# Kernel optimization log

Hardware: AMD Instinct MI355X
Metric: run time of the kernel (lower is better)

Reference implementation:

```python
import jax, jax.numpy as jnp
import numpy as np

F_CONST = 1.0
B_CONST = 0.1
R_CONST = 0.01
N, DIM = 8192, 64


def setup_inputs() -> dict:
    key = jax.random.key(0)
    k1, k2 = jax.random.split(key)
    x = jax.random.uniform(k1, (N, DIM), dtype=jnp.float32)
    A = jax.random.uniform(k2, (N, N), dtype=jnp.float32)
    return {"t": 0, "x": x, "A": A}


def reference(t, x, A):
    # dx_i/dt = f - b*x_i - diag(A @ (r * x x^T))
    # diag(A @ (x x^T))[i] = sum_j A_ij <x_j, x_i> = <x_i, (A x)_i>
    Ax = A @ x                                      # [N, DIM]
    outer = R_CONST * jnp.sum(x * Ax, axis=1, keepdims=True)  # [N, 1]
    return F_CONST - B_CONST * x - outer            # broadcasts to [N, DIM]
```

## Files before the change

### kernel.cpp

```cpp
#include <hip/hip_runtime.h>

#define N 8192
#define DIM 64

typedef float f32x4 __attribute__((ext_vector_type(4)));
typedef short bf16x8 __attribute__((ext_vector_type(8)));

__device__ __forceinline__ unsigned short f32_to_bf16_rne(float f) {
  unsigned int u = __float_as_uint(f);
  unsigned int r = (u + 0x7FFFu + ((u >> 16) & 1u)) >> 16;
  return (unsigned short)r;
}

__global__ void cvt_kernel(const float* __restrict__ x, unsigned short* __restrict__ xb) {
  int gid = blockIdx.x * blockDim.x + threadIdx.x;
  float4 v = reinterpret_cast<const float4*>(x)[gid];
  ushort4 o;
  o.x = f32_to_bf16_rne(v.x);
  o.y = f32_to_bf16_rne(v.y);
  o.z = f32_to_bf16_rne(v.z);
  o.w = f32_to_bf16_rne(v.w);
  reinterpret_cast<ushort4*>(xb)[gid] = o;
}

__global__ void main_kernel(const float* __restrict__ A,
                            const unsigned short* __restrict__ xb,
                            float* __restrict__ spart) {
  int bid = blockIdx.x;
  int rg = bid & 127;
  int js = bid >> 7;
  int tid = threadIdx.x;
  int w = tid >> 6;
  int lane = tid & 63;
  int i0 = rg * 64;
  int jbase = js * 1024 + w * 256;
  int c = lane & 15;
  int q = lane >> 4;

  bf16x8 xi[4][2];
#pragma unroll
  for (int it = 0; it < 4; ++it)
#pragma unroll
    for (int kb = 0; kb < 2; ++kb)
      xi[it][kb] = *reinterpret_cast<const bf16x8*>(
          xb + (size_t)(i0 + it * 16 + c) * DIM + kb * 32 + q * 8);

  float sacc[4][4] = {};

  for (int jt = 0; jt < 16; ++jt) {
    int jcol = jbase + jt * 16;
    bf16x8 xj0 = *reinterpret_cast<const bf16x8*>(
        xb + (size_t)(jcol + c) * DIM + q * 8);
    bf16x8 xj1 = *reinterpret_cast<const bf16x8*>(
        xb + (size_t)(jcol + c) * DIM + 32 + q * 8);

    float a[4][4];
#pragma unroll
    for (int it = 0; it < 4; ++it)
#pragma unroll
      for (int v = 0; v < 4; ++v)
        a[it][v] = A[(size_t)(i0 + it * 16 + q * 4 + v) * N + (jcol + c)];

#pragma unroll
    for (int it = 0; it < 4; ++it) {
      f32x4 g = {0.f, 0.f, 0.f, 0.f};
      g = __builtin_amdgcn_mfma_f32_16x16x32_bf16(xi[it][0], xj0, g, 0, 0, 0);
      g = __builtin_amdgcn_mfma_f32_16x16x32_bf16(xi[it][1], xj1, g, 0, 0, 0);
#pragma unroll
      for (int v = 0; v < 4; ++v)
        sacc[it][v] += a[it][v] * g[v];
    }
  }

#pragma unroll
  for (int it = 0; it < 4; ++it)
#pragma unroll
    for (int v = 0; v < 4; ++v) {
      float s = sacc[it][v];
      s += __shfl_xor(s, 1);
      s += __shfl_xor(s, 2);
      s += __shfl_xor(s, 4);
      s += __shfl_xor(s, 8);
      sacc[it][v] = s;
    }

  __shared__ float red[4][64];
  if (c == 0) {
#pragma unroll
    for (int it = 0; it < 4; ++it)
#pragma unroll
      for (int v = 0; v < 4; ++v)
        red[w][it * 16 + q * 4 + v] = sacc[it][v];
  }
  __syncthreads();
  if (tid < 64) {
    float s = red[0][tid] + red[1][tid] + red[2][tid] + red[3][tid];
    spart[(size_t)js * N + i0 + tid] = s;
  }
}

__global__ void finish_kernel(const float* __restrict__ x,
                              const float* __restrict__ spart,
                              float* __restrict__ out) {
  int gid = blockIdx.x * blockDim.x + threadIdx.x;
  float4 xv = reinterpret_cast<const float4*>(x)[gid];
  int i = gid >> 4;
  float s = 0.f;
#pragma unroll
  for (int cc = 0; cc < 8; ++cc) s += spart[(size_t)cc * N + i];
  float4 o;
  o.x = 1.0f - 0.1f * xv.x - 0.01f * s;
  o.y = 1.0f - 0.1f * xv.y - 0.01f * s;
  o.z = 1.0f - 0.1f * xv.z - 0.01f * s;
  o.w = 1.0f - 0.1f * xv.w - 0.01f * s;
  reinterpret_cast<float4*>(out)[gid] = o;
}

extern "C" void kernel_launch(void* const* d_in, const int* in_sizes, int n_in,
                              void* d_out, int out_size, void* d_ws, size_t ws_size,
                              hipStream_t stream) {
  const float* x = (const float*)d_in[1];
  const float* A = (const float*)d_in[2];
  float* out = (float*)d_out;

  unsigned short* xb = (unsigned short*)d_ws;
  float* spart = (float*)((char*)d_ws + (size_t)N * DIM * 2);

  cvt_kernel<<<512, 256, 0, stream>>>(x, xb);
  main_kernel<<<1024, 256, 0, stream>>>(A, xb, spart);
  finish_kernel<<<512, 256, 0, stream>>>(x, spart, out);
}
```

Baseline: 83.28 us.

## Transpose MFMA operands for float4 A loads and double-buffer the j loop

```diff
diff --git a/kernel.cpp b/kernel.cpp
--- a/kernel.cpp
+++ b/kernel.cpp
@@ -23,9 +23,10 @@
   reinterpret_cast<ushort4*>(xb)[gid] = o;
 }
 
-__global__ void main_kernel(const float* __restrict__ A,
-                            const unsigned short* __restrict__ xb,
-                            float* __restrict__ spart) {
+__global__ __launch_bounds__(256, 4) void main_kernel(
+    const float* __restrict__ A,
+    const unsigned short* __restrict__ xb,
+    float* __restrict__ spart) {
   int bid = blockIdx.x;
   int rg = bid & 127;
   int js = bid >> 7;
@@ -45,52 +46,64 @@
       xi[it][kb] = *reinterpret_cast<const bf16x8*>(
           xb + (size_t)(i0 + it * 16 + c) * DIM + kb * 32 + q * 8);
 
-  float sacc[4][4] = {};
+  const float* pA[4];
+#pragma unroll
+  for (int it = 0; it < 4; ++it)
+    pA[it] = A + (size_t)(i0 + it * 16 + c) * N + jbase + q * 4;
 
+  float sacc[4] = {0.f, 0.f, 0.f, 0.f};
+
+  float4 a_buf[2][4];
+  bf16x8 xj_buf[2][2];
+
+#pragma unroll
+  for (int it = 0; it < 4; ++it)
+    a_buf[0][it] = *reinterpret_cast<const float4*>(pA[it]);
+  {
+    const unsigned short* pj = xb + (size_t)(jbase + c) * DIM + q * 8;
+    xj_buf[0][0] = *reinterpret_cast<const bf16x8*>(pj);
+    xj_buf[0][1] = *reinterpret_cast<const bf16x8*>(pj + 32);
+  }
+
+#pragma unroll
   for (int jt = 0; jt < 16; ++jt) {
-    int jcol = jbase + jt * 16;
-    bf16x8 xj0 = *reinterpret_cast<const bf16x8*>(
-        xb + (size_t)(jcol + c) * DIM + q * 8);
-    bf16x8 xj1 = *reinterpret_cast<const bf16x8*>(
-        xb + (size_t)(jcol + c) * DIM + 32 + q * 8);
-
-    float a[4][4];
+    const int cur = jt & 1, nxt = cur ^ 1;
+    if (jt < 15) {
 #pragma unroll
-    for (int it = 0; it < 4; ++it)
-#pragma unroll
-      for (int v = 0; v < 4; ++v)
-        a[it][v] = A[(size_t)(i0 + it * 16 + q * 4 + v) * N + (jcol + c)];
-
+      for (int it = 0; it < 4; ++it)
+        a_buf[nxt][it] =
+            *reinterpret_cast<const float4*>(pA[it] + (jt + 1) * 16);
+      const unsigned short* pj =
+          xb + (size_t)(jbase + (jt + 1) * 16 + c) * DIM + q * 8;
+      xj_buf[nxt][0] = *reinterpret_cast<const bf16x8*>(pj);
+      xj_buf[nxt][1] = *reinterpret_cast<const bf16x8*>(pj + 32);
+    }
 #pragma unroll
     for (int it = 0; it < 4; ++it) {
       f32x4 g = {0.f, 0.f, 0.f, 0.f};
-      g = __builtin_amdgcn_mfma_f32_16x16x32_bf16(xi[it][0], xj0, g, 0, 0, 0);
-      g = __builtin_amdgcn_mfma_f32_16x16x32_bf16(xi[it][1], xj1, g, 0, 0, 0);
-#pragma unroll
-      for (int v = 0; v < 4; ++v)
-        sacc[it][v] += a[it][v] * g[v];
+      g = __builtin_amdgcn_mfma_f32_16x16x32_bf16(xj_buf[cur][0], xi[it][0], g, 0, 0, 0);
+      g = __builtin_amdgcn_mfma_f32_16x16x32_bf16(xj_buf[cur][1], xi[it][1], g, 0, 0, 0);
+      float4 a4 = a_buf[cur][it];
+      sacc[it] = fmaf(a4.x, g[0], sacc[it]);
+      sacc[it] = fmaf(a4.y, g[1], sacc[it]);
+      sacc[it] = fmaf(a4.z, g[2], sacc[it]);
+      sacc[it] = fmaf(a4.w, g[3], sacc[it]);
     }
   }
 
 #pragma unroll
-  for (int it = 0; it < 4; ++it)
-#pragma unroll
-    for (int v = 0; v < 4; ++v) {
-      float s = sacc[it][v];
-      s += __shfl_xor(s, 1);
-      s += __shfl_xor(s, 2);
-      s += __shfl_xor(s, 4);
-      s += __shfl_xor(s, 8);
-      sacc[it][v] = s;
-    }
+  for (int it = 0; it < 4; ++it) {
+    float s = sacc[it];
+    s += __shfl_xor(s, 16);
+    s += __shfl_xor(s, 32);
+    sacc[it] = s;
+  }
 
   __shared__ float red[4][64];
-  if (c == 0) {
+  if (q == 0) {
 #pragma unroll
     for (int it = 0; it < 4; ++it)
-#pragma unroll
-      for (int v = 0; v < 4; ++v)
-        red[w][it * 16 + q * 4 + v] = sacc[it][v];
+      red[w][it * 16 + c] = sacc[it];
   }
   __syncthreads();
   if (tid < 64) {
```

Result: faster. 75.13 us (-9.8%).

## Restructure Gram-weighted A reduction with vectorized A loads and LDS transpose

Applied to the files above, without the earlier changes.

```diff
diff --git a/kernel.cpp b/kernel.cpp
--- a/kernel.cpp
+++ b/kernel.cpp
@@ -23,79 +23,86 @@
   reinterpret_cast<ushort4*>(xb)[gid] = o;
 }
 
-__global__ void main_kernel(const float* __restrict__ A,
-                            const unsigned short* __restrict__ xb,
-                            float* __restrict__ spart) {
+__global__ __launch_bounds__(256, 4) void main_kernel(
+    const float* __restrict__ A,
+    const unsigned short* __restrict__ xb,
+    float* __restrict__ spart) {
   int bid = blockIdx.x;
   int rg = bid & 127;
   int js = bid >> 7;
   int tid = threadIdx.x;
   int w = tid >> 6;
   int lane = tid & 63;
-  int i0 = rg * 64;
-  int jbase = js * 1024 + w * 256;
+  int i0w = rg * 64 + w * 16;
+  int jbase = js * 1024;
   int c = lane & 15;
   int q = lane >> 4;
+  int h = lane >> 5;
+  int m = lane & 31;
 
-  bf16x8 xi[4][2];
-#pragma unroll
-  for (int it = 0; it < 4; ++it)
-#pragma unroll
-    for (int kb = 0; kb < 2; ++kb)
-      xi[it][kb] = *reinterpret_cast<const bf16x8*>(
-          xb + (size_t)(i0 + it * 16 + c) * DIM + kb * 32 + q * 8);
+  __shared__ alignas(16) float G[4][16][132];
 
-  float sacc[4][4] = {};
+  const unsigned short* pxi = xb + (size_t)(i0w + c) * DIM + q * 8;
+  bf16x8 xi0 = *reinterpret_cast<const bf16x8*>(pxi);
+  bf16x8 xi1 = *reinterpret_cast<const bf16x8*>(pxi + 32);
 
-  for (int jt = 0; jt < 16; ++jt) {
-    int jcol = jbase + jt * 16;
-    bf16x8 xj0 = *reinterpret_cast<const bf16x8*>(
-        xb + (size_t)(jcol + c) * DIM + q * 8);
-    bf16x8 xj1 = *reinterpret_cast<const bf16x8*>(
-        xb + (size_t)(jcol + c) * DIM + 32 + q * 8);
+  float sacc[8] = {0.f, 0.f, 0.f, 0.f, 0.f, 0.f, 0.f, 0.f};
+  f32x4 a_buf[8];
 
-    float a[4][4];
-#pragma unroll
-    for (int it = 0; it < 4; ++it)
-#pragma unroll
-      for (int v = 0; v < 4; ++v)
-        a[it][v] = A[(size_t)(i0 + it * 16 + q * 4 + v) * N + (jcol + c)];
+  const float* pA = A + (size_t)(i0w + h) * N + jbase + m * 4;
 
 #pragma unroll
-    for (int it = 0; it < 4; ++it) {
+  for (int a = 0; a < 8; ++a)
+    a_buf[a] = *reinterpret_cast<const f32x4*>(pA + (size_t)(a * 2) * N);
+
+  for (int cc = 0; cc < 8; ++cc) {
+    int jc = jbase + cc * 128;
+
+#pragma unroll
+    for (int jt = 0; jt < 8; ++jt) {
+      const unsigned short* pj = xb + (size_t)(jc + jt * 16 + c) * DIM + q * 8;
+      bf16x8 xj0 = *reinterpret_cast<const bf16x8*>(pj);
+      bf16x8 xj1 = *reinterpret_cast<const bf16x8*>(pj + 32);
       f32x4 g = {0.f, 0.f, 0.f, 0.f};
-      g = __builtin_amdgcn_mfma_f32_16x16x32_bf16(xi[it][0], xj0, g, 0, 0, 0);
-      g = __builtin_amdgcn_mfma_f32_16x16x32_bf16(xi[it][1], xj1, g, 0, 0, 0);
+      g = __builtin_amdgcn_mfma_f32_16x16x32_bf16(xj0, xi0, g, 0, 0, 0);
+      g = __builtin_amdgcn_mfma_f32_16x16x32_bf16(xj1, xi1, g, 0, 0, 0);
+      *reinterpret_cast<f32x4*>(&G[w][c][jt * 16 + q * 4]) = g;
+    }
+
 #pragma unroll
-      for (int v = 0; v < 4; ++v)
-        sacc[it][v] += a[it][v] * g[v];
+    for (int a = 0; a < 8; ++a) {
+      f32x4 g4 = *reinterpret_cast<const f32x4*>(&G[w][a * 2 + h][m * 4]);
+      f32x4 a4 = a_buf[a];
+      float s = sacc[a];
+      s = fmaf(a4[0], g4[0], s);
+      s = fmaf(a4[1], g4[1], s);
+      s = fmaf(a4[2], g4[2], s);
+      s = fmaf(a4[3], g4[3], s);
+      sacc[a] = s;
+    }
+
+    if (cc < 7) {
+      const float* pAn = pA + (cc + 1) * 128;
+#pragma unroll
+      for (int a = 0; a < 8; ++a)
+        a_buf[a] = *reinterpret_cast<const f32x4*>(pAn + (size_t)(a * 2) * N);
     }
   }
 
 #pragma unroll
-  for (int it = 0; it < 4; ++it)
+  for (int a = 0; a < 8; ++a) {
+    float s = sacc[a];
+    s += __shfl_xor(s, 1);
+    s += __shfl_xor(s, 2);
+    s += __shfl_xor(s, 4);
+    s += __shfl_xor(s, 8);
+    s += __shfl_xor(s, 16);
+    sacc[a] = s;
+  }
+  if (m == 0) {
 #pragma unroll
-    for (int v = 0; v < 4; ++v) {
-      float s = sacc[it][v];
-      s += __shfl_xor(s, 1);
-      s += __shfl_xor(s, 2);
-      s += __shfl_xor(s, 4);
-      s += __shfl_xor(s, 8);
-      sacc[it][v] = s;
-    }
-
-  __shared__ float red[4][64];
-  if (c == 0) {
-#pragma unroll
-    for (int it = 0; it < 4; ++it)
-#pragma unroll
-      for (int v = 0; v < 4; ++v)
-        red[w][it * 16 + q * 4 + v] = sacc[it][v];
-  }
-  __syncthreads();
-  if (tid < 64) {
-    float s = red[0][tid] + red[1][tid] + red[2][tid] + red[3][tid];
-    spart[(size_t)js * N + i0 + tid] = s;
+    for (int a = 0; a < 8; ++a)
+      spart[(size_t)js * N + i0w + a * 2 + h] = sacc[a];
   }
 }
 
```

Measured after the change: 83.71 us. About the same (+0.5%).

## Compute A@x with MFMA directly and stream A through LDS pipeline

Applied to the files above, without the earlier changes.

```diff
diff --git a/kernel.cpp b/kernel.cpp
--- a/kernel.cpp
+++ b/kernel.cpp
@@ -2,118 +2,141 @@
 
 #define N 8192
 #define DIM 64
+#define KS 256
+#define NSUB 32
+#define NBUF 4
 
 typedef float f32x4 __attribute__((ext_vector_type(4)));
 typedef short bf16x8 __attribute__((ext_vector_type(8)));
+typedef unsigned short u16;
 
-__device__ __forceinline__ unsigned short f32_to_bf16_rne(float f) {
+__device__ __forceinline__ u16 f32_to_bf16_rne(float f) {
   unsigned int u = __float_as_uint(f);
-  unsigned int r = (u + 0x7FFFu + ((u >> 16) & 1u)) >> 16;
-  return (unsigned short)r;
+  return (u16)((u + 0x7FFFu + ((u >> 16) & 1u)) >> 16);
 }
 
-__global__ void cvt_kernel(const float* __restrict__ x, unsigned short* __restrict__ xb) {
-  int gid = blockIdx.x * blockDim.x + threadIdx.x;
-  float4 v = reinterpret_cast<const float4*>(x)[gid];
-  ushort4 o;
-  o.x = f32_to_bf16_rne(v.x);
-  o.y = f32_to_bf16_rne(v.y);
-  o.z = f32_to_bf16_rne(v.z);
-  o.w = f32_to_bf16_rne(v.w);
-  reinterpret_cast<ushort4*>(xb)[gid] = o;
+__global__ void cvtT_kernel(const float* __restrict__ x, u16* __restrict__ xbT) {
+  int t = threadIdx.x;
+  int i0 = blockIdx.x * 64;
+  int d = t & 63;
+  int r = t >> 6;
+  int ib = i0 + r * 16;
+  alignas(16) u16 v[16];
+#pragma unroll
+  for (int m = 0; m < 16; ++m)
+    v[m] = f32_to_bf16_rne(x[(size_t)(ib + m) * DIM + d]);
+  *reinterpret_cast<bf16x8*>(xbT + (size_t)d * N + ib) = *reinterpret_cast<bf16x8*>(&v[0]);
+  *reinterpret_cast<bf16x8*>(xbT + (size_t)d * N + ib + 8) = *reinterpret_cast<bf16x8*>(&v[8]);
 }
 
-__global__ void main_kernel(const float* __restrict__ A,
-                            const unsigned short* __restrict__ xb,
-                            float* __restrict__ spart) {
-  int bid = blockIdx.x;
-  int rg = bid & 127;
-  int js = bid >> 7;
+__global__ __launch_bounds__(256, 2) void ax_kernel(const float* __restrict__ A,
+                                                    const u16* __restrict__ xbT,
+                                                    float* __restrict__ Ax) {
+  __shared__ float At[NBUF][16][KS];
+  int i0 = blockIdx.x * 16;
   int tid = threadIdx.x;
-  int w = tid >> 6;
-  int lane = tid & 63;
-  int i0 = rg * 64;
-  int jbase = js * 1024 + w * 256;
-  int c = lane & 15;
-  int q = lane >> 4;
+  int w = tid >> 6, lane = tid & 63;
+  int c = lane & 15, q = lane >> 4;
 
-  bf16x8 xi[4][2];
+  f32x4 acc[4];
 #pragma unroll
-  for (int it = 0; it < 4; ++it)
-#pragma unroll
-    for (int kb = 0; kb < 2; ++kb)
-      xi[it][kb] = *reinterpret_cast<const bf16x8*>(
-          xb + (size_t)(i0 + it * 16 + c) * DIM + kb * 32 + q * 8);
+  for (int nt = 0; nt < 4; ++nt) acc[nt] = (f32x4){0.f, 0.f, 0.f, 0.f};
 
-  float sacc[4][4] = {};
-
-  for (int jt = 0; jt < 16; ++jt) {
-    int jcol = jbase + jt * 16;
-    bf16x8 xj0 = *reinterpret_cast<const bf16x8*>(
-        xb + (size_t)(jcol + c) * DIM + q * 8);
-    bf16x8 xj1 = *reinterpret_cast<const bf16x8*>(
-        xb + (size_t)(jcol + c) * DIM + 32 + q * 8);
-
-    float a[4][4];
-#pragma unroll
-    for (int it = 0; it < 4; ++it)
-#pragma unroll
-      for (int v = 0; v < 4; ++v)
-        a[it][v] = A[(size_t)(i0 + it * 16 + q * 4 + v) * N + (jcol + c)];
-
-#pragma unroll
-    for (int it = 0; it < 4; ++it) {
-      f32x4 g = {0.f, 0.f, 0.f, 0.f};
-      g = __builtin_amdgcn_mfma_f32_16x16x32_bf16(xi[it][0], xj0, g, 0, 0, 0);
-      g = __builtin_amdgcn_mfma_f32_16x16x32_bf16(xi[it][1], xj1, g, 0, 0, 0);
-#pragma unroll
-      for (int v = 0; v < 4; ++v)
-        sacc[it][v] += a[it][v] * g[v];
-    }
+#define STAGE(s_)                                                                   \
+  {                                                                                 \
+    int buf_ = (s_) & (NBUF - 1);                                                   \
+    _Pragma("unroll") for (int rr = 0; rr < 4; ++rr) {                              \
+      int row_ = w * 4 + rr;                                                        \
+      const float* gp_ = A + (size_t)(i0 + row_) * N + (s_)*KS + lane * 4;          \
+      __builtin_amdgcn_global_load_lds(                                             \
+          (const __attribute__((address_space(1))) unsigned int*)gp_,               \
+          (__attribute__((address_space(3))) unsigned int*)&At[buf_][row_][0],      \
+          16, 0, 0);                                                                \
+    }                                                                               \
   }
 
+  STAGE(0); STAGE(1); STAGE(2);
+
+  for (int s = 0; s < NSUB; ++s) {
+    if (s < NSUB - 3) {
+      STAGE(s + 3);
+      asm volatile("s_waitcnt vmcnt(12)" ::: "memory");
+    } else if (s == NSUB - 3) {
+      asm volatile("s_waitcnt vmcnt(8)" ::: "memory");
+    } else if (s == NSUB - 2) {
+      asm volatile("s_waitcnt vmcnt(4)" ::: "memory");
+    } else {
+      asm volatile("s_waitcnt vmcnt(0)" ::: "memory");
+    }
+    __builtin_amdgcn_sched_barrier(0);
+    __builtin_amdgcn_s_barrier();
+    __builtin_amdgcn_sched_barrier(0);
+
+    int buf = s & (NBUF - 1);
 #pragma unroll
-  for (int it = 0; it < 4; ++it)
+    for (int t2 = 0; t2 < 2; ++t2) {
+      int kk = w * 2 + t2;
+      const float* ap = &At[buf][c][kk * 32 + q * 8];
+      f32x4 alo = *reinterpret_cast<const f32x4*>(ap);
+      f32x4 ahi = *reinterpret_cast<const f32x4*>(ap + 4);
+      bf16x8 afv;
+      afv[0] = (short)f32_to_bf16_rne(alo[0]);
+      afv[1] = (short)f32_to_bf16_rne(alo[1]);
+      afv[2] = (short)f32_to_bf16_rne(alo[2]);
+      afv[3] = (short)f32_to_bf16_rne(alo[3]);
+      afv[4] = (short)f32_to_bf16_rne(ahi[0]);
+      afv[5] = (short)f32_to_bf16_rne(ahi[1]);
+      afv[6] = (short)f32_to_bf16_rne(ahi[2]);
+      afv[7] = (short)f32_to_bf16_rne(ahi[3]);
+      const u16* bp = xbT + (size_t)s * KS + kk * 32 + q * 8;
 #pragma unroll
-    for (int v = 0; v < 4; ++v) {
-      float s = sacc[it][v];
-      s += __shfl_xor(s, 1);
-      s += __shfl_xor(s, 2);
-      s += __shfl_xor(s, 4);
-      s += __shfl_xor(s, 8);
-      sacc[it][v] = s;
+      for (int nt = 0; nt < 4; ++nt) {
+        bf16x8 bfv = *reinterpret_cast<const bf16x8*>(bp + (size_t)(nt * 16 + c) * N);
+        acc[nt] = __builtin_amdgcn_mfma_f32_16x16x32_bf16(afv, bfv, acc[nt], 0, 0, 0);
+      }
     }
+    __builtin_amdgcn_s_barrier();
+    __builtin_amdgcn_sched_barrier(0);
+  }
+#undef STAGE
 
-  __shared__ float red[4][64];
-  if (c == 0) {
+  float* Red = &At[0][0][0];
 #pragma unroll
-    for (int it = 0; it < 4; ++it)
+  for (int nt = 0; nt < 4; ++nt)
 #pragma unroll
-      for (int v = 0; v < 4; ++v)
-        red[w][it * 16 + q * 4 + v] = sacc[it][v];
+    for (int v = 0; v < 4; ++v)
+      Red[(w * 16 + q * 4 + v) * 64 + nt * 16 + c] = acc[nt][v];
+  __syncthreads();
+  int ii = tid >> 4, dq = tid & 15;
+  f32x4 sum = *reinterpret_cast<f32x4*>(&Red[(0 * 16 + ii) * 64 + dq * 4]);
+#pragma unroll
+  for (int ww = 1; ww < 4; ++ww) {
+    f32x4 p = *reinterpret_cast<f32x4*>(&Red[(ww * 16 + ii) * 64 + dq * 4]);
+    sum += p;
   }
-  __syncthreads();
-  if (tid < 64) {
-    float s = red[0][tid] + red[1][tid] + red[2][tid] + red[3][tid];
-    spart[(size_t)js * N + i0 + tid] = s;
-  }
+  *reinterpret_cast<f32x4*>(&Ax[(size_t)(i0 + ii) * 64 + dq * 4]) = sum;
 }
 
 __global__ void finish_kernel(const float* __restrict__ x,
-                              const float* __restrict__ spart,
+                              const float* __restrict__ Ax,
                               float* __restrict__ out) {
-  int gid = blockIdx.x * blockDim.x + threadIdx.x;
-  float4 xv = reinterpret_cast<const float4*>(x)[gid];
-  int i = gid >> 4;
-  float s = 0.f;
-#pragma unroll
-  for (int cc = 0; cc < 8; ++cc) s += spart[(size_t)cc * N + i];
-  float4 o;
-  o.x = 1.0f - 0.1f * xv.x - 0.01f * s;
-  o.y = 1.0f - 0.1f * xv.y - 0.01f * s;
-  o.z = 1.0f - 0.1f * xv.z - 0.01f * s;
-  o.w = 1.0f - 0.1f * xv.w - 0.01f * s;
-  reinterpret_cast<float4*>(out)[gid] = o;
+  int tid = threadIdx.x;
+  int i = blockIdx.x * 16 + (tid >> 4);
+  int dq = tid & 15;
+  size_t base = (size_t)i * DIM + dq * 4;
+  f32x4 xv = *reinterpret_cast<const f32x4*>(x + base);
+  f32x4 av = *reinterpret_cast<const f32x4*>(Ax + base);
+  float p = xv[0] * av[0] + xv[1] * av[1] + xv[2] * av[2] + xv[3] * av[3];
+  p += __shfl_xor(p, 1);
+  p += __shfl_xor(p, 2);
+  p += __shfl_xor(p, 4);
+  p += __shfl_xor(p, 8);
+  f32x4 o;
+  o[0] = 1.0f - 0.1f * xv[0] - 0.01f * p;
+  o[1] = 1.0f - 0.1f * xv[1] - 0.01f * p;
+  o[2] = 1.0f - 0.1f * xv[2] - 0.01f * p;
+  o[3] = 1.0f - 0.1f * xv[3] - 0.01f * p;
+  *reinterpret_cast<f32x4*>(out + base) = o;
 }
 
 extern "C" void kernel_launch(void* const* d_in, const int* in_sizes, int n_in,
@@ -123,10 +146,10 @@
   const float* A = (const float*)d_in[2];
   float* out = (float*)d_out;
 
-  unsigned short* xb = (unsigned short*)d_ws;
-  float* spart = (float*)((char*)d_ws + (size_t)N * DIM * 2);
+  u16* xbT = (u16*)d_ws;
+  float* Ax = (float*)((char*)d_ws + (size_t)2 * 1024 * 1024);
 
-  cvt_kernel<<<512, 256, 0, stream>>>(x, xb);
-  main_kernel<<<1024, 256, 0, stream>>>(A, xb, spart);
-  finish_kernel<<<512, 256, 0, stream>>>(x, spart, out);
+  cvtT_kernel<<<128, 256, 0, stream>>>(x, xbT);
+  ax_kernel<<<512, 256, 0, stream>>>(A, xbT, Ax);
+  finish_kernel<<<512, 256, 0, stream>>>(x, Ax, out);
 }
```

Result: slower. 90.60 us (+8.8%).
